# Optimization experiments

Hardware: AMD Instinct MI355X
Metric: run time of the kernel (lower is better)

The kernel has to match this reference:

```python
import jax, jax.numpy as jnp
import numpy as np

B, T, D = 1, 2048, 2048
H, HD = 16, 128          # n_heads, head_dim
RD = 64                  # rotary_emb_dim
K = 4                    # short conv kernel size
EPS = 1e-5


def setup_inputs() -> dict:
    key = jax.random.key(0)
    ks = jax.random.split(key, 10)
    hidden_states = jax.random.normal(ks[0], (B, T, D), dtype=jnp.float32)
    # standard RoPE tables for the rotary sub-dimension
    inv_freq = 1.0 / (10000.0 ** (jnp.arange(0, RD, 2, dtype=jnp.float32) / RD))  # [RD/2]
    pos = jnp.arange(T, dtype=jnp.float32)
    freqs = pos[:, None] * inv_freq[None, :]          # [T, RD/2]
    emb = jnp.concatenate([freqs, freqs], axis=-1)    # [T, RD]
    cos = jnp.broadcast_to(jnp.cos(emb)[None], (B, T, RD))
    sin = jnp.broadcast_to(jnp.sin(emb)[None], (B, T, RD))
    s = 1.0 / np.sqrt(D)
    return {
        "hidden_states": hidden_states,
        "cos": cos, "sin": sin,
        "Wq": jax.random.normal(ks[1], (D, D), jnp.float32) * s,
        "Wk": jax.random.normal(ks[2], (D, D), jnp.float32) * s,
        "Wv": jax.random.normal(ks[3], (D, D), jnp.float32) * s,
        "Wo": jax.random.normal(ks[4], (D, D), jnp.float32) * s,
        "conv_q_w": jax.random.normal(ks[5], (D, K), jnp.float32) * 0.5,
        "conv_k_w": jax.random.normal(ks[6], (D, K), jnp.float32) * 0.5,
        "conv_v_w": jax.random.normal(ks[7], (D, K), jnp.float32) * 0.5,
        "q_norm_w": jnp.ones((HD,), jnp.float32),
        "k_norm_w": jnp.ones((HD,), jnp.float32),
    }


def _causal_conv_silu(x, w):
    # x: [B,T,D], w: [D,K]; depthwise causal conv (tap K-1 hits current pos) + SiLU
    xp = jnp.pad(x, ((0, 0), (K - 1, 0), (0, 0)))
    y = sum(xp[:, j:j + T, :] * w[None, None, :, j] for j in range(K))
    return jax.nn.silu(y)


def _rms_norm(x, w):
    # x: [..., HD]
    var = jnp.mean(x * x, axis=-1, keepdims=True)
    return x * jax.lax.rsqrt(var + EPS) * w


def _rotate_half(x):
    x1, x2 = x[..., : x.shape[-1] // 2], x[..., x.shape[-1] // 2:]
    return jnp.concatenate([-x2, x1], axis=-1)


def _apply_rope(x, cos, sin):
    # x: [B,H,T,HD]; cos/sin: [B,T,RD] -> unsqueeze head dim; partial rotary branch
    cos = cos[:, None, :, :]
    sin = sin[:, None, :, :]
    x_rot, x_pass = x[..., :RD], x[..., RD:]
    x_rot = x_rot * cos + _rotate_half(x_rot) * sin
    # faithful to source: negates rotated part when rotary_dim != head_dim
    return jnp.concatenate([-x_rot, x_pass], axis=-1)


def reference(hidden_states, cos, sin, Wq, Wk, Wv, Wo,
              conv_q_w, conv_k_w, conv_v_w, q_norm_w, k_norm_w):
    # projections (Linear with bias=False: y = x @ W^T)
    q = hidden_states @ Wq.T
    k = hidden_states @ Wk.T
    v = hidden_states @ Wv.T
    # short causal depthwise conv + SiLU
    q = _causal_conv_silu(q, conv_q_w)
    k = _causal_conv_silu(k, conv_k_w)
    v = _causal_conv_silu(v, conv_v_w)
    # split heads: [B,T,D] -> [B,T,H,HD]
    q = q.reshape(B, T, H, HD)
    k = k.reshape(B, T, H, HD)
    v = v.reshape(B, T, H, HD)
    # per-head RMSNorm, then [B,H,T,HD]
    q = _rms_norm(q, q_norm_w).transpose(0, 2, 1, 3)
    k = _rms_norm(k, k_norm_w).transpose(0, 2, 1, 3)
    v = v.transpose(0, 2, 1, 3)
    # RoPE (partial)
    q = _apply_rope(q, cos, sin)
    k = _apply_rope(k, cos, sin)
    # causal attention
    scale = 1.0 / np.sqrt(HD)
    scores = jnp.einsum('bhqd,bhkd->bhqk', q, k) * scale
    causal = jnp.tril(jnp.ones((T, T), dtype=bool))
    scores = jnp.where(causal[None, None], scores, jnp.float32(-1e30))
    probs = jax.nn.softmax(scores, axis=-1)
    attn = jnp.einsum('bhqk,bhkd->bhqd', probs, v)
    # [B,H,T,HD] -> [B,T,D], output projection
    out = attn.transpose(0, 2, 1, 3).reshape(B, T, D) @ Wo.T
    return out
```

## Files before the change

kernel.cpp:

```cpp
#include <hip/hip_runtime.h>
#include <hip/hip_bf16.h>

#define T_SEQ 2048
#define D_MODEL 2048
#define NH 16
#define HDIM 128
#define RD_ROT 64

typedef __bf16 bf16x8 __attribute__((ext_vector_type(8)));
typedef float f32x4 __attribute__((ext_vector_type(4)));

__device__ __forceinline__ void async_copy16(const __bf16* g, __bf16* l) {
    __builtin_amdgcn_global_load_lds(
        (const __attribute__((address_space(1))) void*)g,
        (__attribute__((address_space(3))) void*)l, 16, 0, 0);
}

__global__ __launch_bounds__(256) void cast_kernel(
    const float* __restrict__ s0, const float* __restrict__ s1, const float* __restrict__ s2,
    const float* __restrict__ s3, const float* __restrict__ s4,
    __bf16* __restrict__ d0, __bf16* __restrict__ d1, __bf16* __restrict__ d2,
    __bf16* __restrict__ d3, __bf16* __restrict__ d4)
{
    const float* s; __bf16* d;
    switch (blockIdx.y) {
        case 0: s = s0; d = d0; break;
        case 1: s = s1; d = d1; break;
        case 2: s = s2; d = d2; break;
        case 3: s = s3; d = d3; break;
        default: s = s4; d = d4; break;
    }
    size_t base = (size_t)blockIdx.x * D_MODEL + (size_t)threadIdx.x * 8;
    f32x4 a = *(const f32x4*)(s + base);
    f32x4 b = *(const f32x4*)(s + base + 4);
    bf16x8 o;
    #pragma unroll
    for (int i = 0; i < 4; i++) { o[i] = (__bf16)a[i]; o[i + 4] = (__bf16)b[i]; }
    *(bf16x8*)(d + base) = o;
}

__global__ __launch_bounds__(256) void gemm_bt_kernel(
    const __bf16* __restrict__ A,
    const __bf16* __restrict__ B0, const __bf16* __restrict__ B1, const __bf16* __restrict__ B2,
    __bf16* __restrict__ C0, __bf16* __restrict__ C1, __bf16* __restrict__ C2)
{
    constexpr int BM = 128, BK = 32, KD = D_MODEL;
    const __bf16* Bm = blockIdx.z == 0 ? B0 : (blockIdx.z == 1 ? B1 : B2);
    __bf16* Cm       = blockIdx.z == 0 ? C0 : (blockIdx.z == 1 ? C1 : C2);

    __shared__ __align__(16) __bf16 As[BM * BK];
    __shared__ __align__(16) __bf16 Bs[BM * BK];

    const int lane = threadIdx.x & 63;
    const int wave = threadIdx.x >> 6;
    const int r15  = lane & 15;
    const int quad = lane >> 4;
    const int bm = blockIdx.x * BM;
    const int bn = blockIdx.y * BM;
    const int wm = (wave >> 1) * 64;
    const int wn = (wave & 1) * 64;

    f32x4 acc[4][4] = {};

    const int srow = wave * 32 + (lane >> 2);
    const int sg   = (lane & 3) ^ ((lane >> 2) & 3);

    for (int k0 = 0; k0 < KD; k0 += BK) {
        async_copy16(A  + (size_t)(bm + srow)      * KD + k0 + sg * 8, &As[wave * 1024]);
        async_copy16(A  + (size_t)(bm + srow + 16) * KD + k0 + sg * 8, &As[wave * 1024 + 512]);
        async_copy16(Bm + (size_t)(bn + srow)      * KD + k0 + sg * 8, &Bs[wave * 1024]);
        async_copy16(Bm + (size_t)(bn + srow + 16) * KD + k0 + sg * 8, &Bs[wave * 1024 + 512]);
        __syncthreads();

        bf16x8 av[4], bv[4];
        #pragma unroll
        for (int mt = 0; mt < 4; mt++)
            av[mt] = *(const bf16x8*)&As[(wm + mt * 16 + r15) * 32 + ((quad ^ (r15 & 3)) << 3)];
        #pragma unroll
        for (int nt = 0; nt < 4; nt++)
            bv[nt] = *(const bf16x8*)&Bs[(wn + nt * 16 + r15) * 32 + ((quad ^ (r15 & 3)) << 3)];
        #pragma unroll
        for (int mt = 0; mt < 4; mt++)
            #pragma unroll
            for (int nt = 0; nt < 4; nt++)
                acc[mt][nt] = __builtin_amdgcn_mfma_f32_16x16x32_bf16(av[mt], bv[nt], acc[mt][nt], 0, 0, 0);
        __syncthreads();
    }

    #pragma unroll
    for (int mt = 0; mt < 4; mt++) {
        #pragma unroll
        for (int r = 0; r < 4; r++) {
            size_t row = bm + wm + mt * 16 + quad * 4 + r;
            #pragma unroll
            for (int nt = 0; nt < 4; nt++) {
                size_t col = bn + wn + nt * 16 + r15;
                Cm[row * D_MODEL + col] = (__bf16)acc[mt][nt][r];
            }
        }
    }
}

__global__ __launch_bounds__(256) void gemm_bt_splitk_kernel(
    const __bf16* __restrict__ A, const __bf16* __restrict__ Bm, float* __restrict__ C)
{
    constexpr int BM = 128, BK = 32, KD = D_MODEL;
    __shared__ __align__(16) __bf16 As[BM * BK];
    __shared__ __align__(16) __bf16 Bs[BM * BK];

    const int lane = threadIdx.x & 63;
    const int wave = threadIdx.x >> 6;
    const int r15  = lane & 15;
    const int quad = lane >> 4;
    const int bm = blockIdx.x * BM;
    const int bn = blockIdx.y * BM;
    const int wm = (wave >> 1) * 64;
    const int wn = (wave & 1) * 64;
    const int kbase = blockIdx.z * (KD / 2);

    f32x4 acc[4][4] = {};
    const int srow = wave * 32 + (lane >> 2);
    const int sg   = (lane & 3) ^ ((lane >> 2) & 3);

    for (int k0 = kbase; k0 < kbase + KD / 2; k0 += BK) {
        async_copy16(A  + (size_t)(bm + srow)      * KD + k0 + sg * 8, &As[wave * 1024]);
        async_copy16(A  + (size_t)(bm + srow + 16) * KD + k0 + sg * 8, &As[wave * 1024 + 512]);
        async_copy16(Bm + (size_t)(bn + srow)      * KD + k0 + sg * 8, &Bs[wave * 1024]);
        async_copy16(Bm + (size_t)(bn + srow + 16) * KD + k0 + sg * 8, &Bs[wave * 1024 + 512]);
        __syncthreads();

        bf16x8 av[4], bv[4];
        #pragma unroll
        for (int mt = 0; mt < 4; mt++)
            av[mt] = *(const bf16x8*)&As[(wm + mt * 16 + r15) * 32 + ((quad ^ (r15 & 3)) << 3)];
        #pragma unroll
        for (int nt = 0; nt < 4; nt++)
            bv[nt] = *(const bf16x8*)&Bs[(wn + nt * 16 + r15) * 32 + ((quad ^ (r15 & 3)) << 3)];
        #pragma unroll
        for (int mt = 0; mt < 4; mt++)
            #pragma unroll
            for (int nt = 0; nt < 4; nt++)
                acc[mt][nt] = __builtin_amdgcn_mfma_f32_16x16x32_bf16(av[mt], bv[nt], acc[mt][nt], 0, 0, 0);
        __syncthreads();
    }

    #pragma unroll
    for (int mt = 0; mt < 4; mt++) {
        #pragma unroll
        for (int r = 0; r < 4; r++) {
            size_t row = bm + wm + mt * 16 + quad * 4 + r;
            #pragma unroll
            for (int nt = 0; nt < 4; nt++) {
                size_t col = bn + wn + nt * 16 + r15;
                atomicAdd(&C[row * D_MODEL + col], acc[mt][nt][r]);
            }
        }
    }
}

__global__ __launch_bounds__(256) void preproc_qk_kernel(
    const __bf16* __restrict__ q_raw, const __bf16* __restrict__ k_raw,
    const float* __restrict__ cwq, const float* __restrict__ cwk,
    const float* __restrict__ qnw, const float* __restrict__ knw,
    const float* __restrict__ cosb, const float* __restrict__ sinb,
    __bf16* __restrict__ q_proc, __bf16* __restrict__ k_proc)
{
    const int t = blockIdx.x;
    const int which = blockIdx.y;
    const __bf16* X = which ? k_raw : q_raw;
    const float*  W = which ? cwk : cwq;
    const float*  nw = which ? knw : qnw;
    __bf16* P = which ? k_proc : q_proc;

    const int tid = threadIdx.x;
    const int c0  = tid * 8;
    const int h   = tid >> 4;
    const int dl0 = (tid & 15) * 8;

    f32x4 wv[8];
    #pragma unroll
    for (int i = 0; i < 8; i++) wv[i] = *(const f32x4*)&W[(c0 + i) * 4];

    float acc[8] = {};
    #pragma unroll
    for (int j = 0; j < 4; j++) {
        int tt = t + j - 3;
        if (tt >= 0) {
            bf16x8 xv = *(const bf16x8*)&X[(size_t)tt * D_MODEL + c0];
            #pragma unroll
            for (int i = 0; i < 8; i++) acc[i] += (float)xv[i] * wv[i][j];
        }
    }
    float sil[8], ss = 0.f;
    #pragma unroll
    for (int i = 0; i < 8; i++) {
        float s = acc[i] / (1.f + __expf(-acc[i]));
        sil[i] = s; ss += s * s;
    }
    #pragma unroll
    for (int off = 1; off < 16; off <<= 1) ss += __shfl_xor(ss, off);
    float inv = rsqrtf(ss * (1.f / 128.f) + 1e-5f);

    f32x4 nv0 = *(const f32x4*)&nw[dl0];
    f32x4 nv1 = *(const f32x4*)&nw[dl0 + 4];
    float yn[8];
    #pragma unroll
    for (int i = 0; i < 8; i++) yn[i] = sil[i] * inv * (i < 4 ? nv0[i] : nv1[i - 4]);

    float partner[8];
    #pragma unroll
    for (int i = 0; i < 8; i++) partner[i] = __shfl_xor(yn[i], 4);

    bf16x8 o;
    if (dl0 < RD_ROT) {
        f32x4 cv0 = *(const f32x4*)&cosb[t * RD_ROT + dl0];
        f32x4 cv1 = *(const f32x4*)&cosb[t * RD_ROT + dl0 + 4];
        f32x4 sv0 = *(const f32x4*)&sinb[t * RD_ROT + dl0];
        f32x4 sv1 = *(const f32x4*)&sinb[t * RD_ROT + dl0 + 4];
        #pragma unroll
        for (int i = 0; i < 8; i++) {
            int dl = dl0 + i;
            float c = i < 4 ? cv0[i] : cv1[i - 4];
            float s = i < 4 ? sv0[i] : sv1[i - 4];
            float rot = (dl < 32) ? -partner[i] : partner[i];
            o[i] = (__bf16)(-(yn[i] * c + rot * s));
        }
    } else {
        #pragma unroll
        for (int i = 0; i < 8; i++) o[i] = (__bf16)yn[i];
    }
    *(bf16x8*)&P[((size_t)h * T_SEQ + t) * HDIM + dl0] = o;
}

__global__ __launch_bounds__(128) void preproc_v_kernel(
    const __bf16* __restrict__ v_raw, const float* __restrict__ cwv,
    __bf16* __restrict__ v_t)
{
    const int t0 = blockIdx.x * 8;
    const int h = blockIdx.y;
    const int dl = threadIdx.x;
    const int d = h * HDIM + dl;

    f32x4 wv = *(const f32x4*)&cwv[d * 4];
    float x[11];
    #pragma unroll
    for (int m = 0; m < 11; m++) {
        int tt = t0 - 3 + m;
        x[m] = (tt >= 0) ? (float)v_raw[(size_t)tt * D_MODEL + d] : 0.f;
    }
    bf16x8 o;
    #pragma unroll
    for (int r = 0; r < 8; r++) {
        float y = x[r] * wv[0] + x[r + 1] * wv[1] + x[r + 2] * wv[2] + x[r + 3] * wv[3];
        o[r] = (__bf16)(y / (1.f + __expf(-y)));
    }
    *(bf16x8*)&v_t[((size_t)h * HDIM + dl) * T_SEQ + t0] = o;
}

__global__ __launch_bounds__(256) void attn_kernel(
    const __bf16* __restrict__ Qp,
    const __bf16* __restrict__ Kp,
    const __bf16* __restrict__ Vt,
    __bf16* __restrict__ Op)
{
    constexpr int TQ = 64, TK = 64;
    __shared__ __align__(16) __bf16 Ks[TK * HDIM];
    __shared__ __align__(16) __bf16 Vs[HDIM * TK];
    __shared__ __align__(16) __bf16 Ps[TQ * TK];

    const int lane = threadIdx.x & 63;
    const int wave = threadIdx.x >> 6;
    const int r15  = lane & 15;
    const int quad = lane >> 4;
    const int h = blockIdx.y;
    const int qi = (blockIdx.y & 8) ? ((int)gridDim.x - 1 - (int)blockIdx.x) : (int)blockIdx.x;
    const int q0 = qi * TQ;

    bf16x8 qf[4];
    const __bf16* qbase = Qp + ((size_t)h * T_SEQ + q0 + wave * 16 + r15) * HDIM;
    #pragma unroll
    for (int s = 0; s < 4; s++) qf[s] = *(const bf16x8*)(qbase + s * 32 + quad * 8);

    f32x4 oacc[8] = {};
    float mrow[4], lrow[4];
    #pragma unroll
    for (int r = 0; r < 4; r++) { mrow[r] = -1e30f; lrow[r] = 0.f; }
    const float scale = 0.08838834764831845f;

    const int ntk = q0 / TK + 1;
    for (int it = 0; it < ntk; it++) {
        const int tk0 = it * TK;
        #pragma unroll
        for (int i = 0; i < 4; i++) {
            int chunk = wave * 4 + i;
            int krow = chunk * 4 + (lane >> 4);
            int kg = (lane & 15) ^ (krow & 15);
            async_copy16(Kp + ((size_t)h * T_SEQ + tk0 + krow) * HDIM + kg * 8, &Ks[chunk * 512]);
            int vrow = chunk * 8 + (lane >> 3);
            int vg = (lane & 7) ^ (vrow & 7);
            async_copy16(Vt + ((size_t)h * HDIM + vrow) * T_SEQ + tk0 + vg * 8, &Vs[chunk * 512]);
        }
        __syncthreads();

        f32x4 sacc[4] = {};
        #pragma unroll
        for (int s = 0; s < 4; s++) {
            #pragma unroll
            for (int nt = 0; nt < 4; nt++) {
                bf16x8 kf = *(const bf16x8*)&Ks[(nt * 16 + r15) * HDIM + (((s * 4 + quad) ^ r15) << 3)];
                sacc[nt] = __builtin_amdgcn_mfma_f32_16x16x32_bf16(qf[s], kf, sacc[nt], 0, 0, 0);
            }
        }

        float sv[4][4], tmax[4];
        #pragma unroll
        for (int r = 0; r < 4; r++) tmax[r] = -1e30f;
        #pragma unroll
        for (int nt = 0; nt < 4; nt++) {
            #pragma unroll
            for (int r = 0; r < 4; r++) {
                int qrow = q0 + wave * 16 + quad * 4 + r;
                int kcol = tk0 + nt * 16 + r15;
                float x = sacc[nt][r] * scale;
                x = (kcol > qrow) ? -1e30f : x;
                sv[nt][r] = x;
                tmax[r] = fmaxf(tmax[r], x);
            }
        }
        #pragma unroll
        for (int r = 0; r < 4; r++) {
            #pragma unroll
            for (int off = 1; off < 16; off <<= 1)
                tmax[r] = fmaxf(tmax[r], __shfl_xor(tmax[r], off));
        }
        float alpha[4], rsum[4];
        #pragma unroll
        for (int r = 0; r < 4; r++) {
            float mn = fmaxf(mrow[r], tmax[r]);
            alpha[r] = __expf(mrow[r] - mn);
            mrow[r] = mn;
            rsum[r] = 0.f;
        }
        float pv[4][4];
        #pragma unroll
        for (int nt = 0; nt < 4; nt++) {
            #pragma unroll
            for (int r = 0; r < 4; r++) {
                float p = __expf(sv[nt][r] - mrow[r]);
                pv[nt][r] = p;
                rsum[r] += p;
            }
        }
        #pragma unroll
        for (int r = 0; r < 4; r++) {
            #pragma unroll
            for (int off = 1; off < 16; off <<= 1) rsum[r] += __shfl_xor(rsum[r], off);
            lrow[r] = lrow[r] * alpha[r] + rsum[r];
        }
        #pragma unroll
        for (int nt = 0; nt < 8; nt++) {
            #pragma unroll
            for (int r = 0; r < 4; r++) oacc[nt][r] *= alpha[r];
        }

        #pragma unroll
        for (int nt = 0; nt < 4; nt++) {
            #pragma unroll
            for (int r = 0; r < 4; r++) {
                int prow = wave * 16 + quad * 4 + r;
                int pcol = nt * 16 + r15;
                Ps[prow * TK + ((((pcol >> 3) ^ (prow & 7)) << 3) | (pcol & 7))] = (__bf16)pv[nt][r];
            }
        }

        #pragma unroll
        for (int s = 0; s < 2; s++) {
            bf16x8 pf = *(const bf16x8*)&Ps[(wave * 16 + r15) * TK + (((s * 4 + quad) ^ (r15 & 7)) << 3)];
            #pragma unroll
            for (int nt = 0; nt < 8; nt++) {
                bf16x8 vf = *(const bf16x8*)&Vs[(nt * 16 + r15) * TK + (((s * 4 + quad) ^ (r15 & 7)) << 3)];
                oacc[nt] = __builtin_amdgcn_mfma_f32_16x16x32_bf16(pf, vf, oacc[nt], 0, 0, 0);
            }
        }
        __syncthreads();
    }

    #pragma unroll
    for (int r = 0; r < 4; r++) {
        float inv = 1.0f / lrow[r];
        size_t row = q0 + wave * 16 + quad * 4 + r;
        #pragma unroll
        for (int nt = 0; nt < 8; nt++)
            Op[row * D_MODEL + h * HDIM + nt * 16 + r15] = (__bf16)(oacc[nt][r] * inv);
    }
}

extern "C" void kernel_launch(void* const* d_in, const int* in_sizes, int n_in,
                              void* d_out, int out_size, void* d_ws, size_t ws_size,
                              hipStream_t stream) {
    (void)in_sizes; (void)n_in; (void)out_size; (void)ws_size;
    const float* hidden = (const float*)d_in[0];
    const float* cosb   = (const float*)d_in[1];
    const float* sinb   = (const float*)d_in[2];
    const float* Wq     = (const float*)d_in[3];
    const float* Wk     = (const float*)d_in[4];
    const float* Wv     = (const float*)d_in[5];
    const float* Wo     = (const float*)d_in[6];
    const float* cwq    = (const float*)d_in[7];
    const float* cwk    = (const float*)d_in[8];
    const float* cwv    = (const float*)d_in[9];
    const float* qnw    = (const float*)d_in[10];
    const float* knw    = (const float*)d_in[11];

    const size_t NEL = (size_t)T_SEQ * D_MODEL;
    __bf16* ws = (__bf16*)d_ws;
    __bf16* h_bf   = ws + 0 * NEL;
    __bf16* Wq_bf  = ws + 1 * NEL;
    __bf16* Wk_bf  = ws + 2 * NEL;
    __bf16* Wv_bf  = ws + 3 * NEL;
    __bf16* Wo_bf  = ws + 4 * NEL;
    __bf16* q_raw  = ws + 5 * NEL;
    __bf16* k_raw  = ws + 6 * NEL;
    __bf16* v_raw  = ws + 7 * NEL;
    __bf16* q_proc = Wq_bf;
    __bf16* k_proc = Wk_bf;
    __bf16* v_t    = Wv_bf;
    __bf16* attn_b = h_bf;
    float*  out    = (float*)d_out;

    cast_kernel<<<dim3(T_SEQ, 5), 256, 0, stream>>>(hidden, Wq, Wk, Wv, Wo,
                                                    h_bf, Wq_bf, Wk_bf, Wv_bf, Wo_bf);
    gemm_bt_kernel<<<dim3(16, 16, 3), 256, 0, stream>>>(
        h_bf, Wq_bf, Wk_bf, Wv_bf, q_raw, k_raw, v_raw);
    preproc_qk_kernel<<<dim3(T_SEQ, 2), 256, 0, stream>>>(
        q_raw, k_raw, cwq, cwk, qnw, knw, cosb, sinb, q_proc, k_proc);
    preproc_v_kernel<<<dim3(T_SEQ / 8, NH), 128, 0, stream>>>(v_raw, cwv, v_t);
    attn_kernel<<<dim3(T_SEQ / 64, NH), 256, 0, stream>>>(q_proc, k_proc, v_t, attn_b);
    hipMemsetAsync(d_out, 0, NEL * sizeof(float), stream);
    gemm_bt_splitk_kernel<<<dim3(16, 16, 2), 256, 0, stream>>>(attn_b, Wo_bf, out);
}
```

Baseline: 348.5 us.

## Restructure attention to read K/V straight from global with two query tiles per wave

The attention kernel now runs 2 waves per block, each handling 32 query rows as two 16-row MFMA tiles. K and V fragments are loaded directly from global memory (relying on cache) instead of being staged in LDS, so the block-wide barriers go away. The causal mask is applied only on the last key tile, and the row-sum reduction moves to the end. The softmax scale is folded into Q during preprocessing, and a sign flip is dropped. This removes LDS copy and sync overhead and reuses each K/V fragment across two query tiles, at the risk of more global/L2 traffic and register pressure.

```diff
diff --git a/kernel.cpp b/kernel.cpp
--- a/kernel.cpp
+++ b/kernel.cpp
@@ -171,6 +171,7 @@
     const float*  W = which ? cwk : cwq;
     const float*  nw = which ? knw : qnw;
     __bf16* P = which ? k_proc : q_proc;
+    const float SC = which ? 1.0f : 0.08838834764831845f;
 
     const int tid = threadIdx.x;
     const int c0  = tid * 8;
@@ -223,11 +224,11 @@
             float c = i < 4 ? cv0[i] : cv1[i - 4];
             float s = i < 4 ? sv0[i] : sv1[i - 4];
             float rot = (dl < 32) ? -partner[i] : partner[i];
-            o[i] = (__bf16)(-(yn[i] * c + rot * s));
+            o[i] = (__bf16)((yn[i] * c + rot * s) * SC);
         }
     } else {
         #pragma unroll
-        for (int i = 0; i < 8; i++) o[i] = (__bf16)yn[i];
+        for (int i = 0; i < 8; i++) o[i] = (__bf16)(yn[i] * SC);
     }
     *(bf16x8*)&P[((size_t)h * T_SEQ + t) * HDIM + dl0] = o;
 }
@@ -257,16 +258,14 @@
     *(bf16x8*)&v_t[((size_t)h * HDIM + dl) * T_SEQ + t0] = o;
 }
 
-__global__ __launch_bounds__(256) void attn_kernel(
+__global__ __launch_bounds__(128, 2) void attn_kernel(
     const __bf16* __restrict__ Qp,
     const __bf16* __restrict__ Kp,
     const __bf16* __restrict__ Vt,
     __bf16* __restrict__ Op)
 {
-    constexpr int TQ = 64, TK = 64;
-    __shared__ __align__(16) __bf16 Ks[TK * HDIM];
-    __shared__ __align__(16) __bf16 Vs[HDIM * TK];
-    __shared__ __align__(16) __bf16 Ps[TQ * TK];
+    constexpr int TK = 64, PSTR = 72;
+    __shared__ __align__(16) __bf16 Ps[64 * PSTR];
 
     const int lane = threadIdx.x & 63;
     const int wave = threadIdx.x >> 6;
@@ -274,124 +273,121 @@
     const int quad = lane >> 4;
     const int h = blockIdx.y;
     const int qi = (blockIdx.y & 8) ? ((int)gridDim.x - 1 - (int)blockIdx.x) : (int)blockIdx.x;
-    const int q0 = qi * TQ;
-
-    bf16x8 qf[4];
-    const __bf16* qbase = Qp + ((size_t)h * T_SEQ + q0 + wave * 16 + r15) * HDIM;
-    #pragma unroll
-    for (int s = 0; s < 4; s++) qf[s] = *(const bf16x8*)(qbase + s * 32 + quad * 8);
-
-    f32x4 oacc[8] = {};
-    float mrow[4], lrow[4];
-    #pragma unroll
-    for (int r = 0; r < 4; r++) { mrow[r] = -1e30f; lrow[r] = 0.f; }
-    const float scale = 0.08838834764831845f;
-
-    const int ntk = q0 / TK + 1;
+    const int q0 = qi * 64;
+    const int m0 = wave * 32;
+
+    bf16x8 qf[2][4];
+    #pragma unroll
+    for (int mt = 0; mt < 2; mt++) {
+        const __bf16* qb = Qp + ((size_t)h * T_SEQ + q0 + m0 + mt * 16 + r15) * HDIM + quad * 8;
+        #pragma unroll
+        for (int s = 0; s < 4; s++) qf[mt][s] = *(const bf16x8*)(qb + s * 32);
+    }
+
+    const __bf16* Kb = Kp + (size_t)h * T_SEQ * HDIM;
+    const __bf16* Vb = Vt + (size_t)h * HDIM * T_SEQ;
+
+    f32x4 oacc[2][8] = {};
+    float mrow[2][4], lsum[2][4];
+    #pragma unroll
+    for (int mt = 0; mt < 2; mt++)
+        #pragma unroll
+        for (int r = 0; r < 4; r++) { mrow[mt][r] = -1e30f; lsum[mt][r] = 0.f; }
+
+    const int ntk = qi + 1;
     for (int it = 0; it < ntk; it++) {
         const int tk0 = it * TK;
-        #pragma unroll
-        for (int i = 0; i < 4; i++) {
-            int chunk = wave * 4 + i;
-            int krow = chunk * 4 + (lane >> 4);
-            int kg = (lane & 15) ^ (krow & 15);
-            async_copy16(Kp + ((size_t)h * T_SEQ + tk0 + krow) * HDIM + kg * 8, &Ks[chunk * 512]);
-            int vrow = chunk * 8 + (lane >> 3);
-            int vg = (lane & 7) ^ (vrow & 7);
-            async_copy16(Vt + ((size_t)h * HDIM + vrow) * T_SEQ + tk0 + vg * 8, &Vs[chunk * 512]);
-        }
-        __syncthreads();
-
-        f32x4 sacc[4] = {};
+        const bool last = (it == ntk - 1);
+
+        f32x4 sacc[2][4] = {};
         #pragma unroll
         for (int s = 0; s < 4; s++) {
-            #pragma unroll
-            for (int nt = 0; nt < 4; nt++) {
-                bf16x8 kf = *(const bf16x8*)&Ks[(nt * 16 + r15) * HDIM + (((s * 4 + quad) ^ r15) << 3)];
-                sacc[nt] = __builtin_amdgcn_mfma_f32_16x16x32_bf16(qf[s], kf, sacc[nt], 0, 0, 0);
+            bf16x8 kf[4];
+            #pragma unroll
+            for (int nt = 0; nt < 4; nt++)
+                kf[nt] = *(const bf16x8*)(Kb + (size_t)(tk0 + nt * 16 + r15) * HDIM + s * 32 + quad * 8);
+            #pragma unroll
+            for (int nt = 0; nt < 4; nt++)
+                #pragma unroll
+                for (int mt = 0; mt < 2; mt++)
+                    sacc[mt][nt] = __builtin_amdgcn_mfma_f32_16x16x32_bf16(qf[mt][s], kf[nt], sacc[mt][nt], 0, 0, 0);
+        }
+
+        float alpha[2][4];
+        #pragma unroll
+        for (int mt = 0; mt < 2; mt++) {
+            #pragma unroll
+            for (int r = 0; r < 4; r++) {
+                if (last) {
+                    int qrow = q0 + m0 + mt * 16 + quad * 4 + r;
+                    #pragma unroll
+                    for (int nt = 0; nt < 4; nt++) {
+                        int kcol = tk0 + nt * 16 + r15;
+                        if (kcol > qrow) sacc[mt][nt][r] = -1e30f;
+                    }
+                }
+                float tm = fmaxf(fmaxf(sacc[mt][0][r], sacc[mt][1][r]),
+                                 fmaxf(sacc[mt][2][r], sacc[mt][3][r]));
+                #pragma unroll
+                for (int off = 1; off < 16; off <<= 1) tm = fmaxf(tm, __shfl_xor(tm, off));
+                float mn = fmaxf(mrow[mt][r], tm);
+                float a = __expf(mrow[mt][r] - mn);
+                mrow[mt][r] = mn;
+                alpha[mt][r] = a;
+                float ps = 0.f;
+                #pragma unroll
+                for (int nt = 0; nt < 4; nt++) {
+                    float p = __expf(sacc[mt][nt][r] - mn);
+                    sacc[mt][nt][r] = p;
+                    ps += p;
+                }
+                lsum[mt][r] = lsum[mt][r] * a + ps;
             }
         }
-
-        float sv[4][4], tmax[4];
-        #pragma unroll
-        for (int r = 0; r < 4; r++) tmax[r] = -1e30f;
-        #pragma unroll
-        for (int nt = 0; nt < 4; nt++) {
-            #pragma unroll
-            for (int r = 0; r < 4; r++) {
-                int qrow = q0 + wave * 16 + quad * 4 + r;
-                int kcol = tk0 + nt * 16 + r15;
-                float x = sacc[nt][r] * scale;
-                x = (kcol > qrow) ? -1e30f : x;
-                sv[nt][r] = x;
-                tmax[r] = fmaxf(tmax[r], x);
+        #pragma unroll
+        for (int mt = 0; mt < 2; mt++)
+            #pragma unroll
+            for (int nt = 0; nt < 8; nt++)
+                #pragma unroll
+                for (int r = 0; r < 4; r++) oacc[mt][nt][r] *= alpha[mt][r];
+
+        #pragma unroll
+        for (int mt = 0; mt < 2; mt++)
+            #pragma unroll
+            for (int nt = 0; nt < 4; nt++)
+                #pragma unroll
+                for (int r = 0; r < 4; r++)
+                    Ps[(m0 + mt * 16 + quad * 4 + r) * PSTR + nt * 16 + r15] = (__bf16)sacc[mt][nt][r];
+
+        #pragma unroll
+        for (int s2 = 0; s2 < 2; s2++) {
+            bf16x8 pf[2];
+            #pragma unroll
+            for (int mt = 0; mt < 2; mt++)
+                pf[mt] = *(const bf16x8*)&Ps[(m0 + mt * 16 + r15) * PSTR + s2 * 32 + quad * 8];
+            #pragma unroll
+            for (int nt = 0; nt < 8; nt++) {
+                bf16x8 vf = *(const bf16x8*)(Vb + (size_t)(nt * 16 + r15) * T_SEQ + tk0 + s2 * 32 + quad * 8);
+                #pragma unroll
+                for (int mt = 0; mt < 2; mt++)
+                    oacc[mt][nt] = __builtin_amdgcn_mfma_f32_16x16x32_bf16(pf[mt], vf, oacc[mt][nt], 0, 0, 0);
             }
         }
+    }
+
+    #pragma unroll
+    for (int mt = 0; mt < 2; mt++) {
         #pragma unroll
         for (int r = 0; r < 4; r++) {
-            #pragma unroll
-            for (int off = 1; off < 16; off <<= 1)
-                tmax[r] = fmaxf(tmax[r], __shfl_xor(tmax[r], off));
-        }
-        float alpha[4], rsum[4];
-        #pragma unroll
-        for (int r = 0; r < 4; r++) {
-            float mn = fmaxf(mrow[r], tmax[r]);
-            alpha[r] = __expf(mrow[r] - mn);
-            mrow[r] = mn;
-            rsum[r] = 0.f;
-        }
-        float pv[4][4];
-        #pragma unroll
-        for (int nt = 0; nt < 4; nt++) {
-            #pragma unroll
-            for (int r = 0; r < 4; r++) {
-                float p = __expf(sv[nt][r] - mrow[r]);
-                pv[nt][r] = p;
-                rsum[r] += p;
-            }
-        }
-        #pragma unroll
-        for (int r = 0; r < 4; r++) {
-            #pragma unroll
-            for (int off = 1; off < 16; off <<= 1) rsum[r] += __shfl_xor(rsum[r], off);
-            lrow[r] = lrow[r] * alpha[r] + rsum[r];
-        }
-        #pragma unroll
-        for (int nt = 0; nt < 8; nt++) {
-            #pragma unroll
-            for (int r = 0; r < 4; r++) oacc[nt][r] *= alpha[r];
-        }
-
-        #pragma unroll
-        for (int nt = 0; nt < 4; nt++) {
-            #pragma unroll
-            for (int r = 0; r < 4; r++) {
-                int prow = wave * 16 + quad * 4 + r;
-                int pcol = nt * 16 + r15;
-                Ps[prow * TK + ((((pcol >> 3) ^ (prow & 7)) << 3) | (pcol & 7))] = (__bf16)pv[nt][r];
-            }
-        }
-
-        #pragma unroll
-        for (int s = 0; s < 2; s++) {
-            bf16x8 pf = *(const bf16x8*)&Ps[(wave * 16 + r15) * TK + (((s * 4 + quad) ^ (r15 & 7)) << 3)];
-            #pragma unroll
-            for (int nt = 0; nt < 8; nt++) {
-                bf16x8 vf = *(const bf16x8*)&Vs[(nt * 16 + r15) * TK + (((s * 4 + quad) ^ (r15 & 7)) << 3)];
-                oacc[nt] = __builtin_amdgcn_mfma_f32_16x16x32_bf16(pf, vf, oacc[nt], 0, 0, 0);
-            }
-        }
-        __syncthreads();
-    }
-
-    #pragma unroll
-    for (int r = 0; r < 4; r++) {
-        float inv = 1.0f / lrow[r];
-        size_t row = q0 + wave * 16 + quad * 4 + r;
-        #pragma unroll
-        for (int nt = 0; nt < 8; nt++)
-            Op[row * D_MODEL + h * HDIM + nt * 16 + r15] = (__bf16)(oacc[nt][r] * inv);
+            float l = lsum[mt][r];
+            #pragma unroll
+            for (int off = 1; off < 16; off <<= 1) l += __shfl_xor(l, off);
+            float inv = 1.0f / l;
+            size_t row = q0 + m0 + mt * 16 + quad * 4 + r;
+            #pragma unroll
+            for (int nt = 0; nt < 8; nt++)
+                Op[row * D_MODEL + h * HDIM + nt * 16 + r15] = (__bf16)(oacc[mt][nt][r] * inv);
+        }
     }
 }
 
@@ -435,7 +431,7 @@
     preproc_qk_kernel<<<dim3(T_SEQ, 2), 256, 0, stream>>>(
         q_raw, k_raw, cwq, cwk, qnw, knw, cosb, sinb, q_proc, k_proc);
     preproc_v_kernel<<<dim3(T_SEQ / 8, NH), 128, 0, stream>>>(v_raw, cwv, v_t);
-    attn_kernel<<<dim3(T_SEQ / 64, NH), 256, 0, stream>>>(q_proc, k_proc, v_t, attn_b);
+    attn_kernel<<<dim3(T_SEQ / 64, NH), 128, 0, stream>>>(q_proc, k_proc, v_t, attn_b);
     hipMemsetAsync(d_out, 0, NEL * sizeof(float), stream);
     gemm_bt_splitk_kernel<<<dim3(16, 16, 2), 256, 0, stream>>>(attn_b, Wo_bf, out);
 }
```

Result: slower. 467.8 us (+34.3%).
